# Optimization experiments

Hardware: AMD Instinct MI355X
Metric: run time of the kernel (lower is better)

## Reference

```python
import jax, jax.numpy as jnp
import numpy as np

B, S, D = 4, 2048, 1024  # batch, seq_len, d_model == d_internal


def setup_inputs() -> dict:
    key = jax.random.key(0)
    ks = jax.random.split(key, 7)
    s = 1.0 / np.sqrt(D)  # scale weights so softmax / relu stay in a sane range
    return {
        "input_vecs": jax.random.normal(ks[0], (B, S, D), jnp.float32),
        "Wq": jax.random.normal(ks[1], (D, D), jnp.float32) * s,
        "Wk": jax.random.normal(ks[2], (D, D), jnp.float32) * s,
        "Wv": jax.random.normal(ks[3], (D, D), jnp.float32) * s,
        "W1": jax.random.normal(ks[4], (D, D), jnp.float32) * s,  # linear1: d_internal -> d_model
        "b1": jnp.zeros((D,), jnp.float32),
        "W2": jax.random.normal(ks[5], (D, D), jnp.float32) * s,  # linear2: d_model -> d_internal
        "b2": jnp.zeros((D,), jnp.float32),
    }


def reference(input_vecs, Wq, Wk, Wv, W1, b1, W2, b2):
    d_internal = Wq.shape[1]
    # single-head self-attention: Q,K,V = X @ Wq/Wk/Wv
    q = jnp.einsum("bsd,de->bse", input_vecs, Wq)
    k = jnp.einsum("bsd,de->bse", input_vecs, Wk)
    v = jnp.einsum("bsd,de->bse", input_vecs, Wv)
    scores = jnp.einsum("bqe,bke->bqk", q, k) / jnp.sqrt(jnp.asarray(d_internal, q.dtype))
    attn = jax.nn.softmax(scores, axis=-1)               # [B, S, S]
    attn_out = jnp.einsum("bqk,bke->bqe", attn, v)       # [B, S, D]
    h = attn_out + input_vecs                            # residual 1
    h = jax.nn.relu(h @ W1 + b1)                         # linear1 + relu
    out = h @ W2 + b2 + input_vecs                       # linear2 + residual 2
    return out, attn
```

## Files before the change

kernel.cpp:

```cpp
#include <hip/hip_runtime.h>
#include <hip/hip_bf16.h>

typedef unsigned short u16;
typedef unsigned int   u32;
typedef u16   u16x8 __attribute__((ext_vector_type(8)));
typedef u16   u16x4 __attribute__((ext_vector_type(4)));
typedef __bf16 bf16x8 __attribute__((ext_vector_type(8)));
typedef float f32x4 __attribute__((ext_vector_type(4)));

__device__ __forceinline__ u16 f2bf(float f) {
    u32 u = __float_as_uint(f);
    u = u + 0x7FFFu + ((u >> 16) & 1u);
    return (u16)(u >> 16);
}

__device__ __forceinline__ void gload16(const u16* g, u16* l) {
    __builtin_amdgcn_global_load_lds(
        (const __attribute__((address_space(1))) void*)g,
        (__attribute__((address_space(3))) void*)l,
        16, 0, 0);
}

#define WAITV(N) asm volatile("s_waitcnt vmcnt(" #N ")" ::: "memory")
#define SCHEDB() __builtin_amdgcn_sched_barrier(0)
#define BAR()    __builtin_amdgcn_s_barrier()

__global__ __launch_bounds__(256) void cvt_x(const float* __restrict__ X,
                                             u16* __restrict__ Xb) {
    const long i = (long)(blockIdx.x * 256 + threadIdx.x) * 8;
    float4 a = *(const float4*)(X + i);
    float4 b = *(const float4*)(X + i + 4);
    u16x8 r;
    r[0] = f2bf(a.x); r[1] = f2bf(a.y); r[2] = f2bf(a.z); r[3] = f2bf(a.w);
    r[4] = f2bf(b.x); r[5] = f2bf(b.y); r[6] = f2bf(b.z); r[7] = f2bf(b.w);
    *(u16x8*)(Xb + i) = r;
}

__global__ __launch_bounds__(256) void cvt_wT(const float* __restrict__ w0,
                                              const float* __restrict__ w1,
                                              const float* __restrict__ w2,
                                              const float* __restrict__ w3,
                                              const float* __restrict__ w4,
                                              u16* __restrict__ wt) {
    const float* srcs[5] = {w0, w1, w2, w3, w4};
    const float* W = srcs[blockIdx.z];
    u16* WT = wt + (long)blockIdx.z * 1048576;
    __shared__ float t[32][33];
    const int tx = threadIdx.x, ty = threadIdx.y;
    const int n0 = blockIdx.x * 32, k0 = blockIdx.y * 32;
    #pragma unroll
    for (int r = 0; r < 4; ++r)
        t[ty + 8 * r][tx] = W[(long)(k0 + ty + 8 * r) * 1024 + n0 + tx];
    __syncthreads();
    #pragma unroll
    for (int r = 0; r < 4; ++r)
        WT[(long)(n0 + ty + 8 * r) * 1024 + k0 + tx] = f2bf(t[tx][ty + 8 * r]);
}

enum { EPI_QKV = 0, EPI_SCALE_F32 = 2, EPI_ADDX_BF16 = 3,
       EPI_BIAS_RELU_BF16 = 4, EPI_BIAS_ADDX_F32 = 5 };

#define GBM 256
#define GBN 256
#define GBK 64
#define GSLOT_A (GBM * GBK)
#define GSLOTSZ (2 * GSLOT_A)

template <int EPI>
__global__ __launch_bounds__(512, 2)
void gemm_big(const u16* __restrict__ A, const u16* __restrict__ Bt,
              void* __restrict__ Cout, void* __restrict__ CoutK,
              void* __restrict__ CoutV,
              const int N, const int K,
              const long sA, const long sB, const long sC,
              const float scale) {
    const int GX = gridDim.x, GY = gridDim.y;
    const int p  = blockIdx.x + GX * (blockIdx.y + GY * blockIdx.z);
    const int slab = (p & 7) + 8 * (p / (8 * GY));
    const int vy   = (p >> 3) % GY;
    const int vx   = slab % GX;
    const int bz   = slab / GX;

    const u16* Ab = A + (long)bz * sA;
    const u16* Bb = Bt + (long)bz * sB;

    const int tid  = threadIdx.x;
    const int lane = tid & 63;
    const int w    = tid >> 6;
    const int wrg  = (w >> 2) * 128;
    const int wcg  = (w & 3) * 64;
    const int m0   = vx * GBM;
    const int n0   = vy * GBN;

    __shared__ __align__(16) u16 LDS[2 * GSLOTSZ];

    f32x4 acc[8][4] = {};

    const long Kl = K;
    const int schunk = ((lane & 7) ^ (lane >> 3)) * 8;
    const u16* Ag = Ab + (long)(m0 + w * 32 + (lane >> 3)) * Kl + schunk;
    const u16* Bg = Bb + (long)(n0 + w * 32 + (lane >> 3)) * Kl + schunk;

    const int rbase = lane & 15;
    const int rx    = rbase & 7;
    const int q4    = lane >> 4;

    const int dAoff = (w * 32) * GBK;
    const int dBoff = GSLOT_A + (w * 32) * GBK;

    #define GLDA(mi, ks) (*(const bf16x8*)(Asl + (wrg + (mi) * 16 + rbase) * GBK \
                          + ((((ks) * 4 + q4) ^ rx)) * 8))
    #define GLDB(ni, ks) (*(const bf16x8*)(Bsl + (wcg + (ni) * 16 + rbase) * GBK \
                          + ((((ks) * 4 + q4) ^ rx)) * 8))
    #define GSTAGE_A(KT, D) do {                       \
        gload16(Ag + (KT), (D));                       \
        gload16(Ag + (KT) + 8 * Kl,  (D) + 512);       \
        gload16(Ag + (KT) + 16 * Kl, (D) + 1024);      \
        gload16(Ag + (KT) + 24 * Kl, (D) + 1536);      \
    } while (0)
    #define GSTAGE_B(KT, D) do {                       \
        gload16(Bg + (KT), (D));                       \
        gload16(Bg + (KT) + 8 * Kl,  (D) + 512);       \
        gload16(Bg + (KT) + 16 * Kl, (D) + 1024);      \
        gload16(Bg + (KT) + 24 * Kl, (D) + 1536);      \
    } while (0)
    #define GMFMA2(mi)                                                         \
        _Pragma("unroll")                                                      \
        for (int ni = 0; ni < 4; ++ni) {                                       \
            acc[mi][ni] = __builtin_amdgcn_mfma_f32_16x16x32_bf16(             \
                af0, bf[ni][0], acc[mi][ni], 0, 0, 0);                         \
            acc[mi][ni] = __builtin_amdgcn_mfma_f32_16x16x32_bf16(             \
                af1, bf[ni][1], acc[mi][ni], 0, 0, 0);                         \
        }

    const int nt = K / GBK;
    GSTAGE_A(0, &LDS[0] + dAoff);
    GSTAGE_B(0, &LDS[0] + dBoff);
    WAITV(0);
    BAR();

    for (int t = 0; t < nt; ++t) {
        const int s = t & 1;
        const u16* Asl = &LDS[s * GSLOTSZ];
        const u16* Bsl = &LDS[s * GSLOTSZ] + GSLOT_A;
        u16* dnx = &LDS[(s ^ 1) * GSLOTSZ];
        const bool st = (t + 1 < nt);
        const long kt1 = (long)(t + 1) * GBK;

        bf16x8 bf[4][2], af0, af1;

        if (st) GSTAGE_A(kt1, dnx + dAoff);
        SCHEDB();
        #pragma unroll
        for (int ni = 0; ni < 4; ++ni) {
            bf[ni][0] = GLDB(ni, 0);
            bf[ni][1] = GLDB(ni, 1);
        }
        { af0 = GLDA(0, 0); af1 = GLDA(0, 1); }
        bf16x8 an0 = GLDA(1, 0), an1 = GLDA(1, 1);
        SCHEDB(); BAR();
        __builtin_amdgcn_s_setprio(1);
        GMFMA2(0);
        { af0 = an0; af1 = an1; }
        GMFMA2(1);
        __builtin_amdgcn_s_setprio(0);
        SCHEDB(); BAR();

        if (st) GSTAGE_B(kt1, dnx + dBoff);
        SCHEDB();
        { af0 = GLDA(2, 0); af1 = GLDA(2, 1); }
        an0 = GLDA(3, 0); an1 = GLDA(3, 1);
        SCHEDB(); BAR();
        __builtin_amdgcn_s_setprio(1);
        GMFMA2(2);
        { af0 = an0; af1 = an1; }
        GMFMA2(3);
        __builtin_amdgcn_s_setprio(0);
        SCHEDB(); BAR();

        { af0 = GLDA(4, 0); af1 = GLDA(4, 1); }
        an0 = GLDA(5, 0); an1 = GLDA(5, 1);
        SCHEDB(); BAR();
        __builtin_amdgcn_s_setprio(1);
        GMFMA2(4);
        { af0 = an0; af1 = an1; }
        GMFMA2(5);
        __builtin_amdgcn_s_setprio(0);
        SCHEDB(); BAR();

        { af0 = GLDA(6, 0); af1 = GLDA(6, 1); }
        an0 = GLDA(7, 0); an1 = GLDA(7, 1);
        SCHEDB(); BAR();
        __builtin_amdgcn_s_setprio(1);
        GMFMA2(6);
        { af0 = an0; af1 = an1; }
        GMFMA2(7);
        __builtin_amdgcn_s_setprio(0);
        SCHEDB();
        WAITV(0);
        BAR();
    }
    #undef GLDA
    #undef GLDB
    #undef GSTAGE_A
    #undef GSTAGE_B
    #undef GMFMA2

    const int colb = wcg + (lane & 15);
    const int rq   = (lane >> 4) * 4;
    #pragma unroll
    for (int mi = 0; mi < 8; ++mi) {
        #pragma unroll
        for (int ni = 0; ni < 4; ++ni) {
            f32x4 v = acc[mi][ni];
            const int gr0 = m0 + wrg + mi * 16 + rq;
            const int gc  = n0 + colb + ni * 16;
            if constexpr (EPI == EPI_QKV) {
                if (bz == 2) {
                    u16x4 p2;
                    p2[0] = f2bf(v[0]); p2[1] = f2bf(v[1]);
                    p2[2] = f2bf(v[2]); p2[3] = f2bf(v[3]);
                    u16* C = (u16*)CoutV;
                    const long off = ((long)(gr0 >> 11)) * 2097152 +
                                     (long)gc * 2048 + (gr0 & 2047);
                    *(u16x4*)(C + off) = p2;
                } else {
                    u16* C = (u16*)(bz == 0 ? Cout : CoutK);
                    #pragma unroll
                    for (int j = 0; j < 4; ++j)
                        C[(long)(gr0 + j) * N + gc] = f2bf(v[j]);
                }
            } else if constexpr (EPI == EPI_SCALE_F32) {
                float* C = (float*)Cout + (long)bz * sC;
                #pragma unroll
                for (int j = 0; j < 4; ++j)
                    C[(long)(gr0 + j) * N + gc] = v[j] * scale;
            }
        }
    }
}

#define BM 256
#define BN 128
#define BKW 64
#define SLOT_A (BM * BKW)
#define SLOT_B (BN * BKW)
#define SLOTSZ (SLOT_A + SLOT_B)

template <int EPI>
__global__ __launch_bounds__(512, 1)
void gemm_bt(const u16* __restrict__ A, const u16* __restrict__ Bt,
             void* __restrict__ Cout,
             const float* __restrict__ bias, const float* __restrict__ Xres,
             const int M, const int N, const int K,
             const long sA, const long sB, const long sC, const long sX,
             const float scale) {
    const int GX = gridDim.x, GY = gridDim.y;
    const int p  = blockIdx.x + GX * (blockIdx.y + GY * blockIdx.z);
    const int slab = (p & 7) + 8 * (p / (8 * GY));
    const int vy   = (p >> 3) % GY;
    const int vx   = slab % GX;
    const int vz   = slab / GX;

    const int bz = vz;
    const u16* Ab = A + (long)bz * sA;
    const u16* Bb = Bt + (long)bz * sB;
    const float* Xr = Xres ? Xres + (long)bz * sX : nullptr;

    const int tid  = threadIdx.x;
    const int lane = tid & 63;
    const int w    = tid >> 6;
    const int wrg  = (w >> 1) * 64;
    const int wcg  = (w & 1) * 64;
    const int m0   = vx * BM;
    const int n0   = vy * BN;

    __shared__ __align__(16) u16 LDS[3 * SLOTSZ];

    f32x4 acc[4][4] = {};

    const long Kl = K;
    const int schunk = ((lane & 7) ^ (lane >> 3)) * 8;
    const u16* Ag = Ab + (long)(m0 + w * 32 + (lane >> 3)) * Kl + schunk;
    const u16* Bg = Bb + (long)(n0 + w * 16 + (lane >> 3)) * Kl + schunk;

    const int rbase = lane & 15;
    const int rx    = rbase & 7;
    const int q4    = lane >> 4;

    const int dAoff = (w * 32) * BKW;
    const int dBoff = SLOT_A + (w * 16) * BKW;

    #define LDA(mi, ks) (*(const bf16x8*)(Asl + (wrg + (mi) * 16 + rbase) * BKW \
                         + ((((ks) * 4 + q4) ^ rx)) * 8))
    #define LDB(ni, ks) (*(const bf16x8*)(Bsl + (wcg + (ni) * 16 + rbase) * BKW \
                         + ((((ks) * 4 + q4) ^ rx)) * 8))

    const int nt = K / BKW;
    {
        u16* d0 = &LDS[0];
        gload16(Ag, d0 + dAoff);
        gload16(Ag + 8 * Kl,  d0 + dAoff + 512);
        gload16(Ag + 16 * Kl, d0 + dAoff + 1024);
        gload16(Ag + 24 * Kl, d0 + dAoff + 1536);
        gload16(Bg, d0 + dBoff);
        gload16(Bg + 8 * Kl,  d0 + dBoff + 512);
        u16* d1 = &LDS[SLOTSZ];
        gload16(Ag + BKW, d1 + dAoff);
        gload16(Ag + BKW + 8 * Kl,  d1 + dAoff + 512);
        gload16(Ag + BKW + 16 * Kl, d1 + dAoff + 1024);
        gload16(Ag + BKW + 24 * Kl, d1 + dAoff + 1536);
        gload16(Bg + BKW, d1 + dBoff);
        gload16(Bg + BKW + 8 * Kl,  d1 + dBoff + 512);
    }
    WAITV(6);
    BAR();

    int s = 0;
    for (int t = 0; t < nt; ++t) {
        const u16* Asl = &LDS[s * SLOTSZ];
        const u16* Bsl = &LDS[s * SLOTSZ + SLOT_A];
        const int s2 = (s + 2 >= 3) ? s - 1 : s + 2;
        u16* dA = &LDS[s2 * SLOTSZ] + dAoff;
        u16* dB = &LDS[s2 * SLOTSZ] + dBoff;
        const bool st = (t + 2 < nt);
        const long kt2 = (long)(t + 2) * BKW;

        bf16x8 af[4], bf[4];

        if (st) {
            gload16(Ag + kt2, dA);
            gload16(Ag + kt2 + 8 * Kl, dA + 512);
            gload16(Bg + kt2, dB);
        }
        #pragma unroll
        for (int mi = 0; mi < 4; ++mi) af[mi] = LDA(mi, 0);
        #pragma unroll
        for (int ni = 0; ni < 4; ++ni) bf[ni] = LDB(ni, 0);
        SCHEDB(); BAR();
        __builtin_amdgcn_s_setprio(1);
        #pragma unroll
        for (int mi = 0; mi < 4; ++mi)
            #pragma unroll
            for (int ni = 0; ni < 4; ++ni)
                acc[mi][ni] = __builtin_amdgcn_mfma_f32_16x16x32_bf16(
                    af[mi], bf[ni], acc[mi][ni], 0, 0, 0);
        __builtin_amdgcn_s_setprio(0);
        SCHEDB(); BAR();

        if (st) {
            gload16(Ag + kt2 + 16 * Kl, dA + 1024);
            gload16(Ag + kt2 + 24 * Kl, dA + 1536);
            gload16(Bg + kt2 + 8 * Kl, dB + 512);
        }
        #pragma unroll
        for (int mi = 0; mi < 4; ++mi) af[mi] = LDA(mi, 1);
        #pragma unroll
        for (int ni = 0; ni < 4; ++ni) bf[ni] = LDB(ni, 1);
        SCHEDB(); BAR();
        __builtin_amdgcn_s_setprio(1);
        #pragma unroll
        for (int mi = 0; mi < 4; ++mi)
            #pragma unroll
            for (int ni = 0; ni < 4; ++ni)
                acc[mi][ni] = __builtin_amdgcn_mfma_f32_16x16x32_bf16(
                    af[mi], bf[ni], acc[mi][ni], 0, 0, 0);
        __builtin_amdgcn_s_setprio(0);
        SCHEDB();
        if (st) { WAITV(6); } else { WAITV(0); }
        BAR();

        s = (s == 2) ? 0 : s + 1;
    }
    #undef LDA
    #undef LDB

    const int colb = wcg + (lane & 15);
    const int rq   = (lane >> 4) * 4;
    #pragma unroll
    for (int mi = 0; mi < 4; ++mi) {
        #pragma unroll
        for (int ni = 0; ni < 4; ++ni) {
            f32x4 v = acc[mi][ni];
            const int gr0 = m0 + wrg + mi * 16 + rq;
            const int gc  = n0 + colb + ni * 16;
            #pragma unroll
            for (int j = 0; j < 4; ++j) {
                const long idx = (long)(gr0 + j) * N + gc;
                float val = v[j];
                if constexpr (EPI == EPI_ADDX_BF16) {
                    val += Xr[idx];
                    ((u16*)Cout + (long)bz * sC)[idx] = f2bf(val);
                } else if constexpr (EPI == EPI_BIAS_RELU_BF16) {
                    val = fmaxf(val + bias[gc], 0.0f);
                    ((u16*)Cout + (long)bz * sC)[idx] = f2bf(val);
                } else if constexpr (EPI == EPI_BIAS_ADDX_F32) {
                    ((float*)Cout + (long)bz * sC)[idx] =
                        val + bias[gc] + Xr[idx];
                }
            }
        }
    }
}

__global__ __launch_bounds__(256)
void softmax_rows(float* __restrict__ attn, u16* __restrict__ P) {
    const int row  = blockIdx.x;
    float* rp      = attn + (long)row * 2048;
    const int tid  = threadIdx.x;
    const int lane = tid & 63;
    const int w    = tid >> 6;

    float4 v0 = *(const float4*)(rp + tid * 8);
    float4 v1 = *(const float4*)(rp + tid * 8 + 4);

    float m = fmaxf(fmaxf(fmaxf(v0.x, v0.y), fmaxf(v0.z, v0.w)),
                    fmaxf(fmaxf(v1.x, v1.y), fmaxf(v1.z, v1.w)));
    #pragma unroll
    for (int o = 32; o > 0; o >>= 1) m = fmaxf(m, __shfl_xor(m, o));
    __shared__ float redm[4];
    if (lane == 0) redm[w] = m;
    __syncthreads();
    m = fmaxf(fmaxf(redm[0], redm[1]), fmaxf(redm[2], redm[3]));

    float e[8];
    e[0] = __expf(v0.x - m); e[1] = __expf(v0.y - m);
    e[2] = __expf(v0.z - m); e[3] = __expf(v0.w - m);
    e[4] = __expf(v1.x - m); e[5] = __expf(v1.y - m);
    e[6] = __expf(v1.z - m); e[7] = __expf(v1.w - m);
    float s = ((e[0] + e[1]) + (e[2] + e[3])) + ((e[4] + e[5]) + (e[6] + e[7]));
    #pragma unroll
    for (int o = 32; o > 0; o >>= 1) s += __shfl_xor(s, o);
    __shared__ float reds[4];
    if (lane == 0) reds[w] = s;
    __syncthreads();
    s = (reds[0] + reds[1]) + (reds[2] + reds[3]);
    const float inv = 1.0f / s;

    float4 o0, o1;
    o0.x = e[0] * inv; o0.y = e[1] * inv; o0.z = e[2] * inv; o0.w = e[3] * inv;
    o1.x = e[4] * inv; o1.y = e[5] * inv; o1.z = e[6] * inv; o1.w = e[7] * inv;
    *(float4*)(rp + tid * 8)     = o0;
    *(float4*)(rp + tid * 8 + 4) = o1;

    u16x8 pb;
    pb[0] = f2bf(o0.x); pb[1] = f2bf(o0.y); pb[2] = f2bf(o0.z); pb[3] = f2bf(o0.w);
    pb[4] = f2bf(o1.x); pb[5] = f2bf(o1.y); pb[6] = f2bf(o1.z); pb[7] = f2bf(o1.w);
    *(u16x8*)(P + (long)row * 2048 + tid * 8) = pb;
}

extern "C" void kernel_launch(void* const* d_in, const int* in_sizes, int n_in,
                              void* d_out, int out_size, void* d_ws, size_t ws_size,
                              hipStream_t stream) {
    const float* X  = (const float*)d_in[0];
    const float* Wq = (const float*)d_in[1];
    const float* Wk = (const float*)d_in[2];
    const float* Wv = (const float*)d_in[3];
    const float* W1 = (const float*)d_in[4];
    const float* b1 = (const float*)d_in[5];
    const float* W2 = (const float*)d_in[6];
    const float* b2 = (const float*)d_in[7];

    float* out  = (float*)d_out;
    float* attn = out + (size_t)8388608;

    char* ws = (char*)d_ws;
    u16* Xb  = (u16*)(ws);
    u16* Qb  = (u16*)(ws + (size_t)16 * 1024 * 1024);
    u16* Kb  = (u16*)(ws + (size_t)32 * 1024 * 1024);
    u16* VT  = (u16*)(ws + (size_t)48 * 1024 * 1024);
    u16* H1b = (u16*)(ws + (size_t)64 * 1024 * 1024);
    u16* WTs = (u16*)(ws + (size_t)80 * 1024 * 1024);
    u16* W1T = WTs + (size_t)3 * 1048576;
    u16* W2T = WTs + (size_t)4 * 1048576;
    u16* Pb  = Xb;
    u16* Hb  = Kb;

    cvt_x<<<4096, 256, 0, stream>>>(X, Xb);
    cvt_wT<<<dim3(32, 32, 5), dim3(32, 8), 0, stream>>>(Wq, Wk, Wv, W1, W2, WTs);

    gemm_big<EPI_QKV><<<dim3(32, 4, 3), 512, 0, stream>>>(
        Xb, WTs, Qb, Kb, VT, 1024, 1024, 0, 1048576, 0, 1.0f);

    gemm_big<EPI_SCALE_F32><<<dim3(8, 8, 4), 512, 0, stream>>>(
        Qb, Kb, attn, nullptr, nullptr, 2048, 1024,
        2048L * 1024, 2048L * 1024, 2048L * 2048, 0.03125f);

    softmax_rows<<<8192, 256, 0, stream>>>(attn, Pb);

    gemm_bt<EPI_ADDX_BF16><<<dim3(8, 8, 4), 512, 0, stream>>>(
        Pb, VT, Hb, nullptr, X, 2048, 1024, 2048,
        2048L * 2048, 1024L * 2048, 2048L * 1024, 2048L * 1024, 1.0f);

    gemm_bt<EPI_BIAS_RELU_BF16><<<dim3(32, 8, 1), 512, 0, stream>>>(
        Hb, W1T, H1b, b1, nullptr, 8192, 1024, 1024, 0, 0, 0, 0, 1.0f);

    gemm_bt<EPI_BIAS_ADDX_F32><<<dim3(32, 8, 1), 512, 0, stream>>>(
        H1b, W2T, out, b2, X, 8192, 1024, 1024, 0, 0, 0, 0, 1.0f);
}
```

Baseline: 249.3 us.

## Route QKV GEMM through 256x128 triple-buffered kernel and simplify both GEMM pipelines

The QKV projection moves from the 256x256 double-buffered kernel to the 256x128 triple-buffered gemm_bt kernel, which gets a QKV epilogue. gemm_bt now issues all six loads per stage at once and runs a single 32-MFMA block per K tile, with no mid-iteration barriers or priority hints. gemm_big issues both A and B loads together, software-pipelines A fragment reads across rows, and drops occupancy 2 from its launch bounds. Fewer barriers should lower sync overhead, but removing setprio and the interleaved barriers may hurt overlap of memory and MFMA work.

Result: faster. 243.3 us (-2.4%).

```diff
diff --git a/kernel.cpp b/kernel.cpp
--- a/kernel.cpp
+++ b/kernel.cpp
@@ -60,20 +60,22 @@
 enum { EPI_QKV = 0, EPI_SCALE_F32 = 2, EPI_ADDX_BF16 = 3,
        EPI_BIAS_RELU_BF16 = 4, EPI_BIAS_ADDX_F32 = 5 };
 
-#define GBM 256
-#define GBN 256
-#define GBK 64
-#define GSLOT_A (GBM * GBK)
-#define GSLOTSZ (2 * GSLOT_A)
+#define BM 256
+#define BN 128
+#define BKW 64
+#define SLOT_A (BM * BKW)
+#define SLOT_B (BN * BKW)
+#define SLOTSZ (SLOT_A + SLOT_B)
 
 template <int EPI>
-__global__ __launch_bounds__(512, 2)
-void gemm_big(const u16* __restrict__ A, const u16* __restrict__ Bt,
-              void* __restrict__ Cout, void* __restrict__ CoutK,
-              void* __restrict__ CoutV,
-              const int N, const int K,
-              const long sA, const long sB, const long sC,
-              const float scale) {
+__global__ __launch_bounds__(512, 1)
+void gemm_bt(const u16* __restrict__ A, const u16* __restrict__ Bt,
+             void* __restrict__ Cout, void* __restrict__ CoutK,
+             void* __restrict__ CoutV,
+             const float* __restrict__ bias, const float* __restrict__ Xres,
+             const int M, const int N, const int K,
+             const long sA, const long sB, const long sC, const long sX,
+             const float scale) {
     const int GX = gridDim.x, GY = gridDim.y;
     const int p  = blockIdx.x + GX * (blockIdx.y + GY * blockIdx.z);
     const int slab = (p & 7) + 8 * (p / (8 * GY));
@@ -83,133 +85,109 @@
 
     const u16* Ab = A + (long)bz * sA;
     const u16* Bb = Bt + (long)bz * sB;
+    const float* Xr = Xres ? Xres + (long)bz * sX : nullptr;
 
     const int tid  = threadIdx.x;
     const int lane = tid & 63;
     const int w    = tid >> 6;
-    const int wrg  = (w >> 2) * 128;
-    const int wcg  = (w & 3) * 64;
-    const int m0   = vx * GBM;
-    const int n0   = vy * GBN;
-
-    __shared__ __align__(16) u16 LDS[2 * GSLOTSZ];
-
-    f32x4 acc[8][4] = {};
+    const int wrg  = (w >> 1) * 64;
+    const int wcg  = (w & 1) * 64;
+    const int m0   = vx * BM;
+    const int n0   = vy * BN;
+
+    __shared__ __align__(16) u16 LDS[3 * SLOTSZ];
+
+    f32x4 acc[4][4] = {};
 
     const long Kl = K;
     const int schunk = ((lane & 7) ^ (lane >> 3)) * 8;
     const u16* Ag = Ab + (long)(m0 + w * 32 + (lane >> 3)) * Kl + schunk;
-    const u16* Bg = Bb + (long)(n0 + w * 32 + (lane >> 3)) * Kl + schunk;
+    const u16* Bg = Bb + (long)(n0 + w * 16 + (lane >> 3)) * Kl + schunk;
 
     const int rbase = lane & 15;
     const int rx    = rbase & 7;
     const int q4    = lane >> 4;
 
-    const int dAoff = (w * 32) * GBK;
-    const int dBoff = GSLOT_A + (w * 32) * GBK;
-
-    #define GLDA(mi, ks) (*(const bf16x8*)(Asl + (wrg + (mi) * 16 + rbase) * GBK \
-                          + ((((ks) * 4 + q4) ^ rx)) * 8))
-    #define GLDB(ni, ks) (*(const bf16x8*)(Bsl + (wcg + (ni) * 16 + rbase) * GBK \
-                          + ((((ks) * 4 + q4) ^ rx)) * 8))
-    #define GSTAGE_A(KT, D) do {                       \
-        gload16(Ag + (KT), (D));                       \
-        gload16(Ag + (KT) + 8 * Kl,  (D) + 512);       \
-        gload16(Ag + (KT) + 16 * Kl, (D) + 1024);      \
-        gload16(Ag + (KT) + 24 * Kl, (D) + 1536);      \
-    } while (0)
-    #define GSTAGE_B(KT, D) do {                       \
-        gload16(Bg + (KT), (D));                       \
-        gload16(Bg + (KT) + 8 * Kl,  (D) + 512);       \
-        gload16(Bg + (KT) + 16 * Kl, (D) + 1024);      \
-        gload16(Bg + (KT) + 24 * Kl, (D) + 1536);      \
-    } while (0)
-    #define GMFMA2(mi)                                                         \
-        _Pragma("unroll")                                                      \
-        for (int ni = 0; ni < 4; ++ni) {                                       \
-            acc[mi][ni] = __builtin_amdgcn_mfma_f32_16x16x32_bf16(             \
-                af0, bf[ni][0], acc[mi][ni], 0, 0, 0);                         \
-            acc[mi][ni] = __builtin_amdgcn_mfma_f32_16x16x32_bf16(             \
-                af1, bf[ni][1], acc[mi][ni], 0, 0, 0);                         \
-        }
-
-    const int nt = K / GBK;
-    GSTAGE_A(0, &LDS[0] + dAoff);
-    GSTAGE_B(0, &LDS[0] + dBoff);
-    WAITV(0);
+    const int dAoff = (w * 32) * BKW;
+    const int dBoff = SLOT_A + (w * 16) * BKW;
+
+    #define LDA(mi, ks) (*(const bf16x8*)(Asl + (wrg + (mi) * 16 + rbase) * BKW \
+                         + ((((ks) * 4 + q4) ^ rx)) * 8))
+    #define LDB(ni, ks) (*(const bf16x8*)(Bsl + (wcg + (ni) * 16 + rbase) * BKW \
+                         + ((((ks) * 4 + q4) ^ rx)) * 8))
+
+    const int nt = K / BKW;
+    {
+        u16* d0 = &LDS[0];
+        gload16(Ag, d0 + dAoff);
+        gload16(Ag + 8 * Kl,  d0 + dAoff + 512);
+        gload16(Ag + 16 * Kl, d0 + dAoff + 1024);
+        gload16(Ag + 24 * Kl, d0 + dAoff + 1536);
+        gload16(Bg, d0 + dBoff);
+        gload16(Bg + 8 * Kl,  d0 + dBoff + 512);
+        u16* d1 = &LDS[SLOTSZ];
+        gload16(Ag + BKW, d1 + dAoff);
+        gload16(Ag + BKW + 8 * Kl,  d1 + dAoff + 512);
+        gload16(Ag + BKW + 16 * Kl, d1 + dAoff + 1024);
+        gload16(Ag + BKW + 24 * Kl, d1 + dAoff + 1536);
+        gload16(Bg + BKW, d1 + dBoff);
+        gload16(Bg + BKW + 8 * Kl,  d1 + dBoff + 512);
+    }
+    WAITV(6);
     BAR();
 
+    int s = 0;
     for (int t = 0; t < nt; ++t) {
-        const int s = t & 1;
-        const u16* Asl = &LDS[s * GSLOTSZ];
-        const u16* Bsl = &LDS[s * GSLOTSZ] + GSLOT_A;
-        u16* dnx = &LDS[(s ^ 1) * GSLOTSZ];
-        const bool st = (t + 1 < nt);
-        const long kt1 = (long)(t + 1) * GBK;
-
-        bf16x8 bf[4][2], af0, af1;
-
-        if (st) GSTAGE_A(kt1, dnx + dAoff);
+        const u16* Asl = &LDS[s * SLOTSZ];
+        const u16* Bsl = &LDS[s * SLOTSZ + SLOT_A];
+        const int s2 = (s + 2 >= 3) ? s - 1 : s + 2;
+        u16* dA = &LDS[s2 * SLOTSZ] + dAoff;
+        u16* dB = &LDS[s2 * SLOTSZ] + dBoff;
+        const bool st = (t + 2 < nt);
+        const long kt2 = (long)(t + 2) * BKW;
+
+        if (st) {
+            gload16(Ag + kt2, dA);
+            gload16(Ag + kt2 + 8 * Kl,  dA + 512);
+            gload16(Ag + kt2 + 16 * Kl, dA + 1024);
+            gload16(Ag + kt2 + 24 * Kl, dA + 1536);
+            gload16(Bg + kt2, dB);
+            gload16(Bg + kt2 + 8 * Kl,  dB + 512);
+        }
+
+        bf16x8 af[4][2], bf[4][2];
+        #pragma unroll
+        for (int mi = 0; mi < 4; ++mi) {
+            af[mi][0] = LDA(mi, 0);
+            af[mi][1] = LDA(mi, 1);
+        }
+        #pragma unroll
+        for (int ni = 0; ni < 4; ++ni) {
+            bf[ni][0] = LDB(ni, 0);
+            bf[ni][1] = LDB(ni, 1);
+        }
+        #pragma unroll
+        for (int ks = 0; ks < 2; ++ks)
+            #pragma unroll
+            for (int mi = 0; mi < 4; ++mi)
+                #pragma unroll
+                for (int ni = 0; ni < 4; ++ni)
+                    acc[mi][ni] = __builtin_amdgcn_mfma_f32_16x16x32_bf16(
+                        af[mi][ks], bf[ni][ks], acc[mi][ni], 0, 0, 0);
+
         SCHEDB();
-        #pragma unroll
-        for (int ni = 0; ni < 4; ++ni) {
-            bf[ni][0] = GLDB(ni, 0);
-            bf[ni][1] = GLDB(ni, 1);
-        }
-        { af0 = GLDA(0, 0); af1 = GLDA(0, 1); }
-        bf16x8 an0 = GLDA(1, 0), an1 = GLDA(1, 1);
-        SCHEDB(); BAR();
-        __builtin_amdgcn_s_setprio(1);
-        GMFMA2(0);
-        { af0 = an0; af1 = an1; }
-        GMFMA2(1);
-        __builtin_amdgcn_s_setprio(0);
-        SCHEDB(); BAR();
-
-        if (st) GSTAGE_B(kt1, dnx + dBoff);
+        if (st) { WAITV(6); } else { WAITV(0); }
+        BAR();
         SCHEDB();
-        { af0 = GLDA(2, 0); af1 = GLDA(2, 1); }
-        an0 = GLDA(3, 0); an1 = GLDA(3, 1);
-        SCHEDB(); BAR();
-        __builtin_amdgcn_s_setprio(1);
-        GMFMA2(2);
-        { af0 = an0; af1 = an1; }
-        GMFMA2(3);
-        __builtin_amdgcn_s_setprio(0);
-        SCHEDB(); BAR();
-
-        { af0 = GLDA(4, 0); af1 = GLDA(4, 1); }
-        an0 = GLDA(5, 0); an1 = GLDA(5, 1);
-        SCHEDB(); BAR();
-        __builtin_amdgcn_s_setprio(1);
-        GMFMA2(4);
-        { af0 = an0; af1 = an1; }
-        GMFMA2(5);
-        __builtin_amdgcn_s_setprio(0);
-        SCHEDB(); BAR();
-
-        { af0 = GLDA(6, 0); af1 = GLDA(6, 1); }
-        an0 = GLDA(7, 0); an1 = GLDA(7, 1);
-        SCHEDB(); BAR();
-        __builtin_amdgcn_s_setprio(1);
-        GMFMA2(6);
-        { af0 = an0; af1 = an1; }
-        GMFMA2(7);
-        __builtin_amdgcn_s_setprio(0);
-        SCHEDB();
-        WAITV(0);
-        BAR();
+        s = (s == 2) ? 0 : s + 1;
     }
-    #undef GLDA
-    #undef GLDB
-    #undef GSTAGE_A
-    #undef GSTAGE_B
-    #undef GMFMA2
+    #undef LDA
+    #undef LDB
 
     const int colb = wcg + (lane & 15);
     const int rq   = (lane >> 4) * 4;
     #pragma unroll
-    for (int mi = 0; mi < 8; ++mi) {
+    for (int mi = 0; mi < 4; ++mi) {
         #pragma unroll
         for (int ni = 0; ni < 4; ++ni) {
             f32x4 v = acc[mi][ni];
@@ -230,174 +208,154 @@
                     for (int j = 0; j < 4; ++j)
                         C[(long)(gr0 + j) * N + gc] = f2bf(v[j]);
                 }
-            } else if constexpr (EPI == EPI_SCALE_F32) {
-                float* C = (float*)Cout + (long)bz * sC;
+            } else {
                 #pragma unroll
-                for (int j = 0; j < 4; ++j)
-                    C[(long)(gr0 + j) * N + gc] = v[j] * scale;
+                for (int j = 0; j < 4; ++j) {
+                    const long idx = (long)(gr0 + j) * N + gc;
+                    float val = v[j];
+                    if constexpr (EPI == EPI_ADDX_BF16) {
+                        val += Xr[idx];
+                        ((u16*)Cout + (long)bz * sC)[idx] = f2bf(val);
+                    } else if constexpr (EPI == EPI_BIAS_RELU_BF16) {
+                        val = fmaxf(val + bias[gc], 0.0f);
+                        ((u16*)Cout + (long)bz * sC)[idx] = f2bf(val);
+                    } else if constexpr (EPI == EPI_BIAS_ADDX_F32) {
+                        ((float*)Cout + (long)bz * sC)[idx] =
+                            val + bias[gc] + Xr[idx];
+                    }
+                }
             }
         }
     }
 }
 
-#define BM 256
-#define BN 128
-#define BKW 64
-#define SLOT_A (BM * BKW)
-#define SLOT_B (BN * BKW)
-#define SLOTSZ (SLOT_A + SLOT_B)
+#define GBM 256
+#define GBN 256
+#define GBK 64
+#define GSLOT_A (GBM * GBK)
+#define GSLOTSZ (2 * GSLOT_A)
 
 template <int EPI>
 __global__ __launch_bounds__(512, 1)
-void gemm_bt(const u16* __restrict__ A, const u16* __restrict__ Bt,
-             void* __restrict__ Cout,
-             const float* __restrict__ bias, const float* __restrict__ Xres,
-             const int M, const int N, const int K,
-             const long sA, const long sB, const long sC, const long sX,
-             const float scale) {
+void gemm_big(const u16* __restrict__ A, const u16* __restrict__ Bt,
+              void* __restrict__ Cout,
+              const int N, const int K,
+              const long sA, const long sB, const long sC,
+              const float scale) {
     const int GX = gridDim.x, GY = gridDim.y;
     const int p  = blockIdx.x + GX * (blockIdx.y + GY * blockIdx.z);
     const int slab = (p & 7) + 8 * (p / (8 * GY));
     const int vy   = (p >> 3) % GY;
     const int vx   = slab % GX;
-    const int vz   = slab / GX;
-
-    const int bz = vz;
+    const int bz   = slab / GX;
+
     const u16* Ab = A + (long)bz * sA;
     const u16* Bb = Bt + (long)bz * sB;
-    const float* Xr = Xres ? Xres + (long)bz * sX : nullptr;
 
     const int tid  = threadIdx.x;
     const int lane = tid & 63;
     const int w    = tid >> 6;
-    const int wrg  = (w >> 1) * 64;
-    const int wcg  = (w & 1) * 64;
-    const int m0   = vx * BM;
-    const int n0   = vy * BN;
-
-    __shared__ __align__(16) u16 LDS[3 * SLOTSZ];
-
-    f32x4 acc[4][4] = {};
+    const int wrg  = (w >> 2) * 128;
+    const int wcg  = (w & 3) * 64;
+    const int m0   = vx * GBM;
+    const int n0   = vy * GBN;
+
+    __shared__ __align__(16) u16 LDS[2 * GSLOTSZ];
+
+    f32x4 acc[8][4] = {};
 
     const long Kl = K;
     const int schunk = ((lane & 7) ^ (lane >> 3)) * 8;
     const u16* Ag = Ab + (long)(m0 + w * 32 + (lane >> 3)) * Kl + schunk;
-    const u16* Bg = Bb + (long)(n0 + w * 16 + (lane >> 3)) * Kl + schunk;
+    const u16* Bg = Bb + (long)(n0 + w * 32 + (lane >> 3)) * Kl + schunk;
 
     const int rbase = lane & 15;
     const int rx    = rbase & 7;
     const int q4    = lane >> 4;
 
-    const int dAoff = (w * 32) * BKW;
-    const int dBoff = SLOT_A + (w * 16) * BKW;
-
-    #define LDA(mi, ks) (*(const bf16x8*)(Asl + (wrg + (mi) * 16 + rbase) * BKW \
-                         + ((((ks) * 4 + q4) ^ rx)) * 8))
-    #define LDB(ni, ks) (*(const bf16x8*)(Bsl + (wcg + (ni) * 16 + rbase) * BKW \
-                         + ((((ks) * 4 + q4) ^ rx)) * 8))
-
-    const int nt = K / BKW;
-    {
-        u16* d0 = &LDS[0];
-        gload16(Ag, d0 + dAoff);
-        gload16(Ag + 8 * Kl,  d0 + dAoff + 512);
-        gload16(Ag + 16 * Kl, d0 + dAoff + 1024);
-        gload16(Ag + 24 * Kl, d0 + dAoff + 1536);
-        gload16(Bg, d0 + dBoff);
-        gload16(Bg + 8 * Kl,  d0 + dBoff + 512);
-        u16* d1 = &LDS[SLOTSZ];
-        gload16(Ag + BKW, d1 + dAoff);
-        gload16(Ag + BKW + 8 * Kl,  d1 + dAoff + 512);
-        gload16(Ag + BKW + 16 * Kl, d1 + dAoff + 1024);
-        gload16(Ag + BKW + 24 * Kl, d1 + dAoff + 1536);
-        gload16(Bg + BKW, d1 + dBoff);
-        gload16(Bg + BKW + 8 * Kl,  d1 + dBoff + 512);
+    const int dAoff = (w * 32) * GBK;
+    const int dBoff = GSLOT_A + (w * 32) * GBK;
+
+    #define GLDA(mi, ks) (*(const bf16x8*)(Asl + (wrg + (mi) * 16 + rbase) * GBK \
+                          + ((((ks) * 4 + q4) ^ rx)) * 8))
+    #define GLDB(ni, ks) (*(const bf16x8*)(Bsl + (wcg + (ni) * 16 + rbase) * GBK \
+                          + ((((ks) * 4 + q4) ^ rx)) * 8))
+    #define GSTAGE_A(KT, D) do {                       \
+        gload16(Ag + (KT), (D));                       \
+        gload16(Ag + (KT) + 8 * Kl,  (D) + 512);       \
+        gload16(Ag + (KT) + 16 * Kl, (D) + 1024);      \
+        gload16(Ag + (KT) + 24 * Kl, (D) + 1536);      \
+    } while (0)
+    #define GSTAGE_B(KT, D) do {                       \
+        gload16(Bg + (KT), (D));                       \
+        gload16(Bg + (KT) + 8 * Kl,  (D) + 512);       \
+        gload16(Bg + (KT) + 16 * Kl, (D) + 1024);      \
+        gload16(Bg + (KT) + 24 * Kl, (D) + 1536);      \
+    } while (0)
+
+    const int nt = K / GBK;
+    GSTAGE_A(0, &LDS[0] + dAoff);
+    GSTAGE_B(0, &LDS[0] + dBoff);
+    WAITV(0);
+    BAR();
+
+    for (int t = 0; t < nt; ++t) {
+        const int s = t & 1;
+        const u16* Asl = &LDS[s * GSLOTSZ];
+        const u16* Bsl = &LDS[s * GSLOTSZ] + GSLOT_A;
+        u16* dnx = &LDS[(s ^ 1) * GSLOTSZ];
+        const bool st = (t + 1 < nt);
+        const long kt1 = (long)(t + 1) * GBK;
+
+        if (st) {
+            GSTAGE_A(kt1, dnx + dAoff);
+            GSTAGE_B(kt1, dnx + dBoff);
+        }
+
+        bf16x8 bf[4][2];
+        #pragma unroll
+        for (int ni = 0; ni < 4; ++ni) {
+            bf[ni][0] = GLDB(ni, 0);
+            bf[ni][1] = GLDB(ni, 1);
+        }
+        bf16x8 a0 = GLDA(0, 0), a1 = GLDA(0, 1);
+        #pragma unroll
+        for (int mi = 0; mi < 8; ++mi) {
+            bf16x8 c0 = a0, c1 = a1;
+            if (mi < 7) { a0 = GLDA(mi + 1, 0); a1 = GLDA(mi + 1, 1); }
+            #pragma unroll
+            for (int ni = 0; ni < 4; ++ni) {
+                acc[mi][ni] = __builtin_amdgcn_mfma_f32_16x16x32_bf16(
+                    c0, bf[ni][0], acc[mi][ni], 0, 0, 0);
+                acc[mi][ni] = __builtin_amdgcn_mfma_f32_16x16x32_bf16(
+                    c1, bf[ni][1], acc[mi][ni], 0, 0, 0);
+            }
+        }
+
+        SCHEDB();
+        WAITV(0);
+        BAR();
+        SCHEDB();
     }
-    WAITV(6);
-    BAR();
-
-    int s = 0;
-    for (int t = 0; t < nt; ++t) {
-        const u16* Asl = &LDS[s * SLOTSZ];
-        const u16* Bsl = &LDS[s * SLOTSZ + SLOT_A];
-        const int s2 = (s + 2 >= 3) ? s - 1 : s + 2;
-        u16* dA = &LDS[s2 * SLOTSZ] + dAoff;
-        u16* dB = &LDS[s2 * SLOTSZ] + dBoff;
-        const bool st = (t + 2 < nt);
-        const long kt2 = (long)(t + 2) * BKW;
-
-        bf16x8 af[4], bf[4];
-
-        if (st) {
-            gload16(Ag + kt2, dA);
-            gload16(Ag + kt2 + 8 * Kl, dA + 512);
-            gload16(Bg + kt2, dB);
-        }
-        #pragma unroll
-        for (int mi = 0; mi < 4; ++mi) af[mi] = LDA(mi, 0);
-        #pragma unroll
-        for (int ni = 0; ni < 4; ++ni) bf[ni] = LDB(ni, 0);
-        SCHEDB(); BAR();
-        __builtin_amdgcn_s_setprio(1);
-        #pragma unroll
-        for (int mi = 0; mi < 4; ++mi)
-            #pragma unroll
-            for (int ni = 0; ni < 4; ++ni)
-                acc[mi][ni] = __builtin_amdgcn_mfma_f32_16x16x32_bf16(
-                    af[mi], bf[ni], acc[mi][ni], 0, 0, 0);
-        __builtin_amdgcn_s_setprio(0);
-        SCHEDB(); BAR();
-
-        if (st) {
-            gload16(Ag + kt2 + 16 * Kl, dA + 1024);
-            gload16(Ag + kt2 + 24 * Kl, dA + 1536);
-            gload16(Bg + kt2 + 8 * Kl, dB + 512);
-        }
-        #pragma unroll
-        for (int mi = 0; mi < 4; ++mi) af[mi] = LDA(mi, 1);
-        #pragma unroll
-        for (int ni = 0; ni < 4; ++ni) bf[ni] = LDB(ni, 1);
-        SCHEDB(); BAR();
-        __builtin_amdgcn_s_setprio(1);
-        #pragma unroll
-        for (int mi = 0; mi < 4; ++mi)
-            #pragma unroll
-            for (int ni = 0; ni < 4; ++ni)
-                acc[mi][ni] = __builtin_amdgcn_mfma_f32_16x16x32_bf16(
-                    af[mi], bf[ni], acc[mi][ni], 0, 0, 0);
-        __builtin_amdgcn_s_setprio(0);
-        SCHEDB();
-        if (st) { WAITV(6); } else { WAITV(0); }
-        BAR();
-
-        s = (s == 2) ? 0 : s + 1;
-    }
-    #undef LDA
-    #undef LDB
+    #undef GLDA
+    #undef GLDB
+    #undef GSTAGE_A
+    #undef GSTAGE_B
 
     const int colb = wcg + (lane & 15);
     const int rq   = (lane >> 4) * 4;
     #pragma unroll
-    for (int mi = 0; mi < 4; ++mi) {
+    for (int mi = 0; mi < 8; ++mi) {
         #pragma unroll
         for (int ni = 0; ni < 4; ++ni) {
             f32x4 v = acc[mi][ni];
             const int gr0 = m0 + wrg + mi * 16 + rq;
             const int gc  = n0 + colb + ni * 16;
-            #pragma unroll
-            for (int j = 0; j < 4; ++j) {
-                const long idx = (long)(gr0 + j) * N + gc;
-                float val = v[j];
-                if constexpr (EPI == EPI_ADDX_BF16) {
-                    val += Xr[idx];
-                    ((u16*)Cout + (long)bz * sC)[idx] = f2bf(val);
-                } else if constexpr (EPI == EPI_BIAS_RELU_BF16) {
-                    val = fmaxf(val + bias[gc], 0.0f);
-                    ((u16*)Cout + (long)bz * sC)[idx] = f2bf(val);
-                } else if constexpr (EPI == EPI_BIAS_ADDX_F32) {
-                    ((float*)Cout + (long)bz * sC)[idx] =
-                        val + bias[gc] + Xr[idx];
-                }
+            if constexpr (EPI == EPI_SCALE_F32) {
+                float* C = (float*)Cout + (long)bz * sC;
+                #pragma unroll
+                for (int j = 0; j < 4; ++j)
+                    C[(long)(gr0 + j) * N + gc] = v[j] * scale;
             }
         }
     }
@@ -479,22 +437,25 @@
     cvt_x<<<4096, 256, 0, stream>>>(X, Xb);
     cvt_wT<<<dim3(32, 32, 5), dim3(32, 8), 0, stream>>>(Wq, Wk, Wv, W1, W2, WTs);
 
-    gemm_big<EPI_QKV><<<dim3(32, 4, 3), 512, 0, stream>>>(
-        Xb, WTs, Qb, Kb, VT, 1024, 1024, 0, 1048576, 0, 1.0f);
+    gemm_bt<EPI_QKV><<<dim3(32, 8, 3), 512, 0, stream>>>(
+        Xb, WTs, Qb, Kb, VT, nullptr, nullptr, 8192, 1024, 1024,
+        0, 1048576, 0, 0, 1.0f);
 
     gemm_big<EPI_SCALE_F32><<<dim3(8, 8, 4), 512, 0, stream>>>(
-        Qb, Kb, attn, nullptr, nullptr, 2048, 1024,
+        Qb, Kb, attn, 2048, 1024,
         2048L * 1024, 2048L * 1024, 2048L * 2048, 0.03125f);
 
     softmax_rows<<<8192, 256, 0, stream>>>(attn, Pb);
 
     gemm_bt<EPI_ADDX_BF16><<<dim3(8, 8, 4), 512, 0, stream>>>(
-        Pb, VT, Hb, nullptr, X, 2048, 1024, 2048,
+        Pb, VT, Hb, nullptr, nullptr, nullptr, X, 2048, 1024, 2048,
         2048L * 2048, 1024L * 2048, 2048L * 1024, 2048L * 1024, 1.0f);
 
     gemm_bt<EPI_BIAS_RELU_BF16><<<dim3(32, 8, 1), 512, 0, stream>>>(
-        Hb, W1T, H1b, b1, nullptr, 8192, 1024, 1024, 0, 0, 0, 0, 1.0f);
+        Hb, W1T, H1b, nullptr, nullptr, b1, nullptr, 8192, 1024, 1024,
+        0, 0, 0, 0, 1.0f);
 
     gemm_bt<EPI_BIAS_ADDX_F32><<<dim3(32, 8, 1), 512, 0, stream>>>(
-        H1b, W2T, out, b2, X, 8192, 1024, 1024, 0, 0, 0, 0, 1.0f);
-}
+        H1b, W2T, out, nullptr, nullptr, b2, X, 8192, 1024, 1024,
+        0, 0, 0, 0, 1.0f);
+}
```
